# Optimization experiments

Hardware: AMD Instinct MI355X
Metric: run time of the kernel (lower is better)

Reference implementation:

```python
import jax, jax.numpy as jnp
import numpy as np

N_NODES = 100000
N_EDGES = 1600000
IN_F = 48
OUT_F = 48


def setup_inputs() -> dict:
    key = jax.random.key(0)
    k1, k2, k3, k4 = jax.random.split(key, 4)
    x = jax.random.normal(k1, (N_NODES, IN_F), dtype=jnp.float32)
    edge_index = jax.random.randint(k2, (2, N_EDGES), 0, N_NODES, dtype=jnp.int32)
    # nn.Linear(in_features, out_features): W is [out, in], b is [out]
    bound = 1.0 / np.sqrt(IN_F)
    W = jax.random.uniform(k3, (OUT_F, IN_F), minval=-bound, maxval=bound, dtype=jnp.float32)
    b = jax.random.uniform(k4, (OUT_F,), minval=-bound, maxval=bound, dtype=jnp.float32)
    return {"x": x, "edge_index": edge_index, "W": W, "b": b}


def reference(x, edge_index, W, b):
    row, col = edge_index[0], edge_index[1]
    n = x.shape[0]
    # degree of each node as message target (bincount over row)
    deg = jnp.bincount(row, length=n).astype(x.dtype)
    deg_inv_sqrt = jnp.where(deg > 0, jax.lax.rsqrt(jnp.where(deg > 0, deg, 1.0)), 0.0)
    norm = deg_inv_sqrt[row] * deg_inv_sqrt[col]          # [E]
    # symmetric-normalized GCN aggregation: sum over edges of norm * x[col] into row
    msg = norm[:, None] * x[col]                           # [E, in]
    agg = jax.ops.segment_sum(msg, row, num_segments=n)    # [N, in]
    out = agg @ W.T + b                                    # [N, out]
    return jax.nn.relu(out)
```

## Files before the change

### kernel.cpp

```cpp
#include <hip/hip_runtime.h>


#define NF 48
#define NPAIR 24
#define ZLD 32
#define RB 64
#define CHUNK 16384
#define SCOL_CAP 2048

typedef __attribute__((ext_vector_type(8))) short frag_ab;
typedef __attribute__((ext_vector_type(4))) float f32x4;

__device__ inline unsigned short f2bf(float f) {
    unsigned u = __float_as_uint(f);
    u = (u + 0x7fffu + ((u >> 16) & 1u)) >> 16;
    return (unsigned short)u;
}

__global__ void transform_kernel(const float* __restrict__ x, const float* __restrict__ W,
                                 const float* __restrict__ dis,
                                 unsigned short* __restrict__ zp16, int N) {
    __shared__ unsigned short Xb[64 * 64];
    __shared__ unsigned short Wb[48 * 64];
    const int tid = threadIdx.x;
    const int nb0 = blockIdx.x * 64;

    const float4* x4 = (const float4*)x;
    for (int i = tid; i < 768; i += 256) {
        int r = i / 12, c = i % 12;
        int n = nb0 + r;
        float4 v = (n < N) ? x4[(size_t)n * 12 + c] : make_float4(0.f, 0.f, 0.f, 0.f);
        unsigned short* d = &Xb[r * 64 + c * 4];
        d[0] = f2bf(v.x); d[1] = f2bf(v.y); d[2] = f2bf(v.z); d[3] = f2bf(v.w);
    }
    for (int i = tid; i < 64 * 8; i += 256)
        ((unsigned*)Xb)[(i >> 3) * 32 + 24 + (i & 7)] = 0u;
    const float4* W4 = (const float4*)W;
    for (int i = tid; i < 576; i += 256) {
        int r = i / 12, c = i % 12;
        float4 v = W4[r * 12 + c];
        unsigned short* d = &Wb[r * 64 + c * 4];
        d[0] = f2bf(v.x); d[1] = f2bf(v.y); d[2] = f2bf(v.z); d[3] = f2bf(v.w);
    }
    for (int i = tid; i < 48 * 8; i += 256)
        ((unsigned*)Wb)[(i >> 3) * 32 + 24 + (i & 7)] = 0u;
    __syncthreads();

    const int wv = tid >> 6, lane = tid & 63;
    const int quad = lane >> 4, l16 = lane & 15;
    const int mrow = wv * 16 + l16;

    frag_ab A0 = *(const frag_ab*)&Xb[mrow * 64 + quad * 8];
    frag_ab A1 = *(const frag_ab*)&Xb[mrow * 64 + 32 + quad * 8];
    f32x4 acc[3];
#pragma unroll
    for (int t = 0; t < 3; t++) {
        frag_ab B0 = *(const frag_ab*)&Wb[(t * 16 + l16) * 64 + quad * 8];
        frag_ab B1 = *(const frag_ab*)&Wb[(t * 16 + l16) * 64 + 32 + quad * 8];
        f32x4 z = {0.f, 0.f, 0.f, 0.f};
        z = __builtin_amdgcn_mfma_f32_16x16x32_bf16(A0, B0, z, 0, 0, 0);
        z = __builtin_amdgcn_mfma_f32_16x16x32_bf16(A1, B1, z, 0, 0, 0);
        acc[t] = z;
    }
#pragma unroll
    for (int r = 0; r < 4; r++) {
        int n = nb0 + wv * 16 + quad * 4 + r;
        if (n < N) {
            float dn = dis[n];
            unsigned short* zr = zp16 + (size_t)n * 64;
#pragma unroll
            for (int t = 0; t < 3; t++)
                zr[t * 16 + l16] = f2bf(dn * acc[t][r]);
            zr[48 + l16] = 0;
        }
    }
}

__global__ void histA_kernel(const int* __restrict__ row, int* __restrict__ blkhist,
                             int NBUK, int E) {
    extern __shared__ int hist[];
    for (int i = threadIdx.x; i < NBUK; i += blockDim.x) hist[i] = 0;
    __syncthreads();
    int b = blockIdx.x;
    int s = b * CHUNK, t = min(E, s + CHUNK);
    int nv = (t - s) >> 2;
    const int4* r4 = (const int4*)(row + s);
    for (int i = threadIdx.x; i < nv; i += blockDim.x) {
        int4 r = r4[i];
        atomicAdd(&hist[r.x >> 6], 1);
        atomicAdd(&hist[r.y >> 6], 1);
        atomicAdd(&hist[r.z >> 6], 1);
        atomicAdd(&hist[r.w >> 6], 1);
    }
    for (int e = s + nv * 4 + threadIdx.x; e < t; e += blockDim.x)
        atomicAdd(&hist[row[e] >> 6], 1);
    __syncthreads();
    int* dst = blkhist + (size_t)b * NBUK;
    for (int k = threadIdx.x; k < NBUK; k += blockDim.x) dst[k] = hist[k];
}

__global__ void scanB1_kernel(int* __restrict__ blkhist, int* __restrict__ btotal,
                              int NBUK, int NCH) {
    int k = blockIdx.x;
    int lane = threadIdx.x;
    int carry = 0;
    for (int base = 0; base < NCH; base += 64) {
        int i = base + lane;
        int v = (i < NCH) ? blkhist[(size_t)i * NBUK + k] : 0;
        int incl = v;
        #pragma unroll
        for (int off = 1; off < 64; off <<= 1) {
            int u = __shfl_up(incl, off, 64);
            if (lane >= off) incl += u;
        }
        if (i < NCH) blkhist[(size_t)i * NBUK + k] = carry + incl - v;
        carry += __shfl(incl, 63, 64);
    }
    if (lane == 0) btotal[k] = carry;
}

__global__ void scanB2_kernel(const int* __restrict__ btotal, int* __restrict__ bbase,
                              int NBUK, int E) {
    __shared__ int wsum[8];
    __shared__ int carry_s;
    if (threadIdx.x == 0) carry_s = 0;
    __syncthreads();
    const int lane = threadIdx.x & 63;
    const int wave = threadIdx.x >> 6;
    for (int base = 0; base < NBUK; base += 512) {
        int i = base + threadIdx.x;
        int v = (i < NBUK) ? btotal[i] : 0;
        int incl = v;
        #pragma unroll
        for (int off = 1; off < 64; off <<= 1) {
            int u = __shfl_up(incl, off, 64);
            if (lane >= off) incl += u;
        }
        if (lane == 63) wsum[wave] = incl;
        __syncthreads();
        int woff = 0;
        #pragma unroll
        for (int w = 0; w < 8; w++) if (w < wave) woff += wsum[w];
        if (i < NBUK) bbase[i] = carry_s + woff + (incl - v);
        __syncthreads();
        if (threadIdx.x == 511) carry_s += woff + incl;
        __syncthreads();
    }
    if (threadIdx.x == 0) bbase[NBUK] = E;
}

__global__ void scatC_kernel(const int* __restrict__ row, const int* __restrict__ col,
                             const int* __restrict__ blkhist, const int* __restrict__ bbase,
                             unsigned* __restrict__ binned, int NBUK, int E) {
    extern __shared__ int cur[];
    int b = blockIdx.x;
    const int* boff = blkhist + (size_t)b * NBUK;
    for (int k = threadIdx.x; k < NBUK; k += blockDim.x)
        cur[k] = bbase[k] + boff[k];
    __syncthreads();
    int s = b * CHUNK, t = min(E, s + CHUNK);
    int nv = (t - s) >> 2;
    const int4* r4 = (const int4*)(row + s);
    const int4* c4 = (const int4*)(col + s);
    for (int i = threadIdx.x; i < nv; i += blockDim.x) {
        int4 r = r4[i];
        int4 c = c4[i];
        int p0 = atomicAdd(&cur[r.x >> 6], 1);
        binned[p0] = ((unsigned)(r.x & (RB - 1)) << 26) | (unsigned)c.x;
        int p1 = atomicAdd(&cur[r.y >> 6], 1);
        binned[p1] = ((unsigned)(r.y & (RB - 1)) << 26) | (unsigned)c.y;
        int p2 = atomicAdd(&cur[r.z >> 6], 1);
        binned[p2] = ((unsigned)(r.z & (RB - 1)) << 26) | (unsigned)c.z;
        int p3 = atomicAdd(&cur[r.w >> 6], 1);
        binned[p3] = ((unsigned)(r.w & (RB - 1)) << 26) | (unsigned)c.w;
    }
    for (int e = s + nv * 4 + threadIdx.x; e < t; e += blockDim.x) {
        int r = row[e], c = col[e];
        int pos = atomicAdd(&cur[r >> 6], 1);
        binned[pos] = ((unsigned)(r & (RB - 1)) << 26) | (unsigned)c;
    }
}

__global__ void degdis_kernel(const int* __restrict__ bbase, const unsigned* __restrict__ binned,
                              float* __restrict__ dis, int* __restrict__ lrp_g, int N) {
    __shared__ int hist[RB];
    const int b = blockIdx.x;
    const int s = bbase[b];
    const int t = bbase[b + 1];
    const int tid = threadIdx.x;
    if (tid < RB) hist[tid] = 0;
    __syncthreads();
    for (int e = s + tid; e < t; e += 512)
        atomicAdd(&hist[binned[e] >> 26], 1);
    __syncthreads();
    if (tid < RB) {
        int v = hist[tid];
        int incl = v;
        #pragma unroll
        for (int off = 1; off < 64; off <<= 1) {
            int u = __shfl_up(incl, off, 64);
            if (tid >= off) incl += u;
        }
        int* lp = lrp_g + (size_t)b * (RB + 1);
        lp[tid] = incl - v;
        if (tid == RB - 1) lp[RB] = incl;
        int n = b * RB + tid;
        if (n < N) dis[n] = (v > 0) ? rsqrtf((float)v) : 0.0f;
    }
}

__global__ __launch_bounds__(512, 8)
void aggregate_kernel(const int* __restrict__ bbase, const unsigned* __restrict__ binned,
                      const int* __restrict__ lrp_g,
                      const unsigned* __restrict__ zp, const float* __restrict__ dis,
                      const float* __restrict__ bias, float* __restrict__ out, int N) {
    __shared__ int scol[SCOL_CAP];
    __shared__ int lrp[RB + 1];
    __shared__ int cur[RB];
    const int b = blockIdx.x;
    const int s = bbase[b];
    const int t = bbase[b + 1];
    const int cnt = t - s;
    const int tid = threadIdx.x;
    if (tid < RB + 1) {
        int v = lrp_g[(size_t)b * (RB + 1) + tid];
        lrp[tid] = v;
        if (tid < RB) cur[tid] = v;
    }
    __syncthreads();
    const bool sorted = (cnt <= SCOL_CAP);
    if (sorted) {
        for (int e = s + tid; e < t; e += 512) {
            unsigned rc = binned[e];
            int pos = atomicAdd(&cur[rc >> 26], 1);
            scol[pos] = (int)(rc & 0x3ffffffu);
        }
    }
    __syncthreads();

    const int lane = tid & 63;
    const int wave = tid >> 6;
    const int h = lane >> 5;
    const int j = lane & 31;
    const bool act = (j < NPAIR);
    float bb0 = 0.0f, bb1 = 0.0f;
    if (act) { bb0 = bias[2 * j]; bb1 = bias[2 * j + 1]; }
    const int rbase = b * RB;
    for (int ri = wave; ri < RB; ri += 8) {
        int r = rbase + ri;
        if (r >= N) break;
        float a0 = 0.0f, a1 = 0.0f;
        if (sorted) {
            int ks = lrp[ri], ke = lrp[ri + 1];
            int k = ks + h;
            for (; k + 6 < ke; k += 8) {
                int c0 = scol[k];
                int c1 = scol[k + 2];
                int c2 = scol[k + 4];
                int c3 = scol[k + 6];
                unsigned u0 = zp[((size_t)c0 << 5) + j];
                unsigned u1 = zp[((size_t)c1 << 5) + j];
                unsigned u2 = zp[((size_t)c2 << 5) + j];
                unsigned u3 = zp[((size_t)c3 << 5) + j];
                a0 += (__uint_as_float(u0 << 16) + __uint_as_float(u1 << 16)) +
                      (__uint_as_float(u2 << 16) + __uint_as_float(u3 << 16));
                a1 += (__uint_as_float(u0 & 0xffff0000u) + __uint_as_float(u1 & 0xffff0000u)) +
                      (__uint_as_float(u2 & 0xffff0000u) + __uint_as_float(u3 & 0xffff0000u));
            }
            for (; k < ke; k += 2) {
                int c0 = scol[k];
                unsigned u0 = zp[((size_t)c0 << 5) + j];
                a0 += __uint_as_float(u0 << 16);
                a1 += __uint_as_float(u0 & 0xffff0000u);
            }
        } else {
            for (int e = s; e < t; e++) {
                unsigned rc = binned[e];
                if ((int)(rc >> 26) == ri && h == 0 && act) {
                    unsigned u0 = zp[((size_t)(rc & 0x3ffffffu) << 5) + j];
                    a0 += __uint_as_float(u0 << 16);
                    a1 += __uint_as_float(u0 & 0xffff0000u);
                }
            }
        }
        a0 += __shfl_xor(a0, 32, 64);
        a1 += __shfl_xor(a1, 32, 64);
        if (h == 0 && act) {
            float dr = dis[r];
            float v0 = dr * a0 + bb0;
            float v1 = dr * a1 + bb1;
            float2 o;
            o.x = v0 > 0.0f ? v0 : 0.0f;
            o.y = v1 > 0.0f ? v1 : 0.0f;
            *(float2*)(out + (size_t)r * NF + 2 * j) = o;
        }
    }
}

extern "C" void kernel_launch(void* const* d_in, const int* in_sizes, int n_in,
                              void* d_out, int out_size, void* d_ws, size_t ws_size,
                              hipStream_t stream) {
    const float* x    = (const float*)d_in[0];
    const int*   ei   = (const int*)d_in[1];
    const float* W    = (const float*)d_in[2];
    const float* bias = (const float*)d_in[3];
    float* out = (float*)d_out;

    const int N = in_sizes[0] / NF;
    const int E = in_sizes[1] / 2;
    const int* row = ei;
    const int* col = ei + E;
    const int NBUK = (N + RB - 1) / RB;
    const int NCH  = (E + CHUNK - 1) / CHUNK;

    char* ws = (char*)d_ws;
    unsigned* zp      = (unsigned*)ws;       ws += (size_t)N * ZLD * 4;
    unsigned* binned  = (unsigned*)ws;       ws += (size_t)E * 4;
    float*    dis     = (float*)ws;          ws += (size_t)N * 4;
    int*      blkhist = (int*)ws;            ws += (size_t)NCH * NBUK * 4;
    int*      btotal  = (int*)ws;            ws += (size_t)NBUK * 4;
    int*      bbase   = (int*)ws;            ws += (size_t)(NBUK + 1) * 4;
    int*      lrp_g   = (int*)ws;            ws += (size_t)NBUK * (RB + 1) * 4;

    histA_kernel<<<NCH, 512, NBUK * 4, stream>>>(row, blkhist, NBUK, E);
    scanB1_kernel<<<NBUK, 64, 0, stream>>>(blkhist, btotal, NBUK, NCH);
    scanB2_kernel<<<1, 512, 0, stream>>>(btotal, bbase, NBUK, E);
    scatC_kernel<<<NCH, 512, NBUK * 4, stream>>>(row, col, blkhist, bbase, binned, NBUK, E);
    degdis_kernel<<<NBUK, 512, 0, stream>>>(bbase, binned, dis, lrp_g, N);
    transform_kernel<<<(N + 63) / 64, 256, 0, stream>>>(x, W, dis, (unsigned short*)zp, N);
    aggregate_kernel<<<NBUK, 512, 0, stream>>>(bbase, binned, lrp_g, zp, dis, bias, out, N);
}
```

Before: 159.3 us.

## Widen aggregate gathers to 8-byte loads and serialize per-bucket column scan

The aggregate kernel now has each lane load a uint2 (four bf16 features), with 16 lanes covering one padded row. That lets four edges be in flight per wave slot instead of two, with a two-step shuffle reduction and float4 output stores. The goal is fewer load instructions, wider memory transactions and better use of lanes, since 12 of 16 lanes are active versus 24 of 32 before. Separately, scanB1 now runs a sequential per-thread scan over chunks with coalesced access across buckets, replacing one wave per bucket doing strided shuffle scans. This uses far fewer blocks but gives a longer serial loop per thread.

```diff
diff --git a/kernel.cpp b/kernel.cpp
--- a/kernel.cpp
+++ b/kernel.cpp
@@ -2,7 +2,6 @@
 
 
 #define NF 48
-#define NPAIR 24
 #define ZLD 32
 #define RB 64
 #define CHUNK 16384
@@ -101,22 +100,16 @@
 
 __global__ void scanB1_kernel(int* __restrict__ blkhist, int* __restrict__ btotal,
                               int NBUK, int NCH) {
-    int k = blockIdx.x;
-    int lane = threadIdx.x;
+    int k = blockIdx.x * 64 + threadIdx.x;
+    if (k >= NBUK) return;
     int carry = 0;
-    for (int base = 0; base < NCH; base += 64) {
-        int i = base + lane;
-        int v = (i < NCH) ? blkhist[(size_t)i * NBUK + k] : 0;
-        int incl = v;
-        #pragma unroll
-        for (int off = 1; off < 64; off <<= 1) {
-            int u = __shfl_up(incl, off, 64);
-            if (lane >= off) incl += u;
-        }
-        if (i < NCH) blkhist[(size_t)i * NBUK + k] = carry + incl - v;
-        carry += __shfl(incl, 63, 64);
-    }
-    if (lane == 0) btotal[k] = carry;
+    for (int i = 0; i < NCH; i++) {
+        int* p = blkhist + (size_t)i * NBUK + k;
+        int v = *p;
+        *p = carry;
+        carry += v;
+    }
+    btotal[k] = carry;
 }
 
 __global__ void scanB2_kernel(const int* __restrict__ btotal, int* __restrict__ bbase,
@@ -212,7 +205,7 @@
 __global__ __launch_bounds__(512, 8)
 void aggregate_kernel(const int* __restrict__ bbase, const unsigned* __restrict__ binned,
                       const int* __restrict__ lrp_g,
-                      const unsigned* __restrict__ zp, const float* __restrict__ dis,
+                      const uint2* __restrict__ zp2, const float* __restrict__ dis,
                       const float* __restrict__ bias, float* __restrict__ out, int N) {
     __shared__ int scol[SCOL_CAP];
     __shared__ int lrp[RB + 1];
@@ -240,59 +233,68 @@
 
     const int lane = tid & 63;
     const int wave = tid >> 6;
-    const int h = lane >> 5;
-    const int j = lane & 31;
-    const bool act = (j < NPAIR);
-    float bb0 = 0.0f, bb1 = 0.0f;
-    if (act) { bb0 = bias[2 * j]; bb1 = bias[2 * j + 1]; }
+    const int slot = lane >> 4;
+    const int q    = lane & 15;
+    float4 bb = make_float4(0.f, 0.f, 0.f, 0.f);
+    if (q < 12) bb = ((const float4*)bias)[q];
     const int rbase = b * RB;
     for (int ri = wave; ri < RB; ri += 8) {
         int r = rbase + ri;
         if (r >= N) break;
-        float a0 = 0.0f, a1 = 0.0f;
+        float a0 = 0.f, a1 = 0.f, a2 = 0.f, a3 = 0.f;
         if (sorted) {
             int ks = lrp[ri], ke = lrp[ri + 1];
-            int k = ks + h;
-            for (; k + 6 < ke; k += 8) {
+            int k = ks + slot;
+            for (; k + 12 < ke; k += 16) {
                 int c0 = scol[k];
-                int c1 = scol[k + 2];
-                int c2 = scol[k + 4];
-                int c3 = scol[k + 6];
-                unsigned u0 = zp[((size_t)c0 << 5) + j];
-                unsigned u1 = zp[((size_t)c1 << 5) + j];
-                unsigned u2 = zp[((size_t)c2 << 5) + j];
-                unsigned u3 = zp[((size_t)c3 << 5) + j];
-                a0 += (__uint_as_float(u0 << 16) + __uint_as_float(u1 << 16)) +
-                      (__uint_as_float(u2 << 16) + __uint_as_float(u3 << 16));
-                a1 += (__uint_as_float(u0 & 0xffff0000u) + __uint_as_float(u1 & 0xffff0000u)) +
-                      (__uint_as_float(u2 & 0xffff0000u) + __uint_as_float(u3 & 0xffff0000u));
+                int c1 = scol[k + 4];
+                int c2 = scol[k + 8];
+                int c3 = scol[k + 12];
+                uint2 u0 = zp2[((size_t)c0 << 4) + q];
+                uint2 u1 = zp2[((size_t)c1 << 4) + q];
+                uint2 u2 = zp2[((size_t)c2 << 4) + q];
+                uint2 u3 = zp2[((size_t)c3 << 4) + q];
+                a0 += (__uint_as_float(u0.x << 16) + __uint_as_float(u1.x << 16)) +
+                      (__uint_as_float(u2.x << 16) + __uint_as_float(u3.x << 16));
+                a1 += (__uint_as_float(u0.x & 0xffff0000u) + __uint_as_float(u1.x & 0xffff0000u)) +
+                      (__uint_as_float(u2.x & 0xffff0000u) + __uint_as_float(u3.x & 0xffff0000u));
+                a2 += (__uint_as_float(u0.y << 16) + __uint_as_float(u1.y << 16)) +
+                      (__uint_as_float(u2.y << 16) + __uint_as_float(u3.y << 16));
+                a3 += (__uint_as_float(u0.y & 0xffff0000u) + __uint_as_float(u1.y & 0xffff0000u)) +
+                      (__uint_as_float(u2.y & 0xffff0000u) + __uint_as_float(u3.y & 0xffff0000u));
             }
-            for (; k < ke; k += 2) {
-                int c0 = scol[k];
-                unsigned u0 = zp[((size_t)c0 << 5) + j];
-                a0 += __uint_as_float(u0 << 16);
-                a1 += __uint_as_float(u0 & 0xffff0000u);
+            for (; k < ke; k += 4) {
+                int c = scol[k];
+                uint2 u = zp2[((size_t)c << 4) + q];
+                a0 += __uint_as_float(u.x << 16);
+                a1 += __uint_as_float(u.x & 0xffff0000u);
+                a2 += __uint_as_float(u.y << 16);
+                a3 += __uint_as_float(u.y & 0xffff0000u);
             }
         } else {
             for (int e = s; e < t; e++) {
                 unsigned rc = binned[e];
-                if ((int)(rc >> 26) == ri && h == 0 && act) {
-                    unsigned u0 = zp[((size_t)(rc & 0x3ffffffu) << 5) + j];
-                    a0 += __uint_as_float(u0 << 16);
-                    a1 += __uint_as_float(u0 & 0xffff0000u);
+                if ((int)(rc >> 26) == ri && slot == 0) {
+                    uint2 u = zp2[((size_t)(rc & 0x3ffffffu) << 4) + q];
+                    a0 += __uint_as_float(u.x << 16);
+                    a1 += __uint_as_float(u.x & 0xffff0000u);
+                    a2 += __uint_as_float(u.y << 16);
+                    a3 += __uint_as_float(u.y & 0xffff0000u);
                 }
             }
         }
-        a0 += __shfl_xor(a0, 32, 64);
-        a1 += __shfl_xor(a1, 32, 64);
-        if (h == 0 && act) {
+        a0 += __shfl_xor(a0, 16, 64); a0 += __shfl_xor(a0, 32, 64);
+        a1 += __shfl_xor(a1, 16, 64); a1 += __shfl_xor(a1, 32, 64);
+        a2 += __shfl_xor(a2, 16, 64); a2 += __shfl_xor(a2, 32, 64);
+        a3 += __shfl_xor(a3, 16, 64); a3 += __shfl_xor(a3, 32, 64);
+        if (slot == 0 && q < 12) {
             float dr = dis[r];
-            float v0 = dr * a0 + bb0;
-            float v1 = dr * a1 + bb1;
-            float2 o;
-            o.x = v0 > 0.0f ? v0 : 0.0f;
-            o.y = v1 > 0.0f ? v1 : 0.0f;
-            *(float2*)(out + (size_t)r * NF + 2 * j) = o;
+            float4 o;
+            o.x = fmaxf(dr * a0 + bb.x, 0.0f);
+            o.y = fmaxf(dr * a1 + bb.y, 0.0f);
+            o.z = fmaxf(dr * a2 + bb.z, 0.0f);
+            o.w = fmaxf(dr * a3 + bb.w, 0.0f);
+            *(float4*)(out + (size_t)r * NF + q * 4) = o;
         }
     }
 }
@@ -323,10 +325,10 @@
     int*      lrp_g   = (int*)ws;            ws += (size_t)NBUK * (RB + 1) * 4;
 
     histA_kernel<<<NCH, 512, NBUK * 4, stream>>>(row, blkhist, NBUK, E);
-    scanB1_kernel<<<NBUK, 64, 0, stream>>>(blkhist, btotal, NBUK, NCH);
+    scanB1_kernel<<<(NBUK + 63) / 64, 64, 0, stream>>>(blkhist, btotal, NBUK, NCH);
     scanB2_kernel<<<1, 512, 0, stream>>>(btotal, bbase, NBUK, E);
     scatC_kernel<<<NCH, 512, NBUK * 4, stream>>>(row, col, blkhist, bbase, binned, NBUK, E);
     degdis_kernel<<<NBUK, 512, 0, stream>>>(bbase, binned, dis, lrp_g, N);
     transform_kernel<<<(N + 63) / 64, 256, 0, stream>>>(x, W, dis, (unsigned short*)zp, N);
-    aggregate_kernel<<<NBUK, 512, 0, stream>>>(bbase, binned, lrp_g, zp, dis, bias, out, N);
-}
+    aggregate_kernel<<<NBUK, 512, 0, stream>>>(bbase, binned, lrp_g, (const uint2*)zp, dis, bias, out, N);
+}
```

New measurement: 178.8 us. 12.2% more time.
